# Performance work log

Measured on AMD Instinct MI355X. Metric: run time of the kernel, lower is better.

## Reference

```python
import jax, jax.numpy as jnp
import numpy as np

N_EMBD = 1024
N_HEAD = 16

def setup_inputs() -> dict:
    key = jax.random.key(0)
    ks = jax.random.split(key, 6)
    C = N_EMBD
    s = 1.0 / np.sqrt(C)
    x = jax.random.normal(ks[0], (4, 2048, C), dtype=jnp.float32)
    Wk = jax.random.normal(ks[1], (C, C), dtype=jnp.float32) * s
    Wq = jax.random.normal(ks[2], (C, C), dtype=jnp.float32) * s
    Wv = jax.random.normal(ks[3], (C, C), dtype=jnp.float32) * s
    Wp = jax.random.normal(ks[4], (C, C), dtype=jnp.float32) * s
    bp = jax.random.normal(ks[5], (C,), dtype=jnp.float32) * 0.01
    return {"x": x, "Wq": Wq, "Wk": Wk, "Wv": Wv, "Wp": Wp, "bp": bp}

def reference(x, Wq, Wk, Wv, Wp, bp):
    B, T, C = x.shape
    H = N_HEAD
    d = C // H
    # projections (bias=False)
    q = (x @ Wq).reshape(B, T, H, d).transpose(0, 2, 1, 3)  # [B,H,T,d]
    k = (x @ Wk).reshape(B, T, H, d).transpose(0, 2, 1, 3)
    v = (x @ Wv).reshape(B, T, H, d).transpose(0, 2, 1, 3)
    att = jnp.einsum('bhqd,bhkd->bhqk', q, k) * (1.0 / np.sqrt(d))
    causal = jnp.tril(jnp.ones((T, T), dtype=bool))
    att = jnp.where(causal[None, None], att, jnp.float32(-jnp.inf))
    att = jax.nn.softmax(att, axis=-1)
    y = jnp.einsum('bhqk,bhkd->bhqd', att, v)  # [B,H,T,d]
    y = y.transpose(0, 2, 1, 3).reshape(B, T, C)
    return y @ Wp + bp
```

## Files before the change

### kernel.cpp

```cpp
#include <hip/hip_runtime.h>
#include <hip/hip_bf16.h>

#define N_EMBD 1024
#define N_HEADS 16
#define HD 64
#define TSEQ 2048
#define BATCH 4
#define M_TOT (BATCH*TSEQ)

typedef short s16x8 __attribute__((ext_vector_type(8)));
typedef float f32x4 __attribute__((ext_vector_type(4)));

__device__ __forceinline__ void glds16(const void* g, void* l) {
  __builtin_amdgcn_global_load_lds((const __attribute__((address_space(1))) void*)g,
                                   (__attribute__((address_space(3))) void*)l, 16, 0, 0);
}

__global__ __launch_bounds__(256) void xcast_kernel(const float* __restrict__ x,
                                                    __hip_bfloat16* __restrict__ xb) {
  int i = blockIdx.x * 256 + threadIdx.x;
  float4 f = ((const float4*)x)[i];
  __hip_bfloat162 p0, p1;
  p0.x = __float2bfloat16(f.x); p0.y = __float2bfloat16(f.y);
  p1.x = __float2bfloat16(f.z); p1.y = __float2bfloat16(f.w);
  ((__hip_bfloat162*)xb)[2*i]   = p0;
  ((__hip_bfloat162*)xb)[2*i+1] = p1;
}

__global__ void wcast_kernel(const float* __restrict__ Wq, const float* __restrict__ Wk,
                             const float* __restrict__ Wv, const float* __restrict__ Wp,
                             __hip_bfloat16* __restrict__ wqkvt, __hip_bfloat16* __restrict__ wpt) {
  __shared__ float tile[32][33];
  int z = blockIdx.z;
  const float* in = (z==0)?Wq:(z==1)?Wk:(z==2)?Wv:Wp;
  __hip_bfloat16* out = (z<3) ? (wqkvt + (size_t)z*N_EMBD*N_EMBD) : wpt;
  int tx = threadIdx.x, ty = threadIdx.y;
  int x  = blockIdx.x*32 + tx;
  int y0 = blockIdx.y*32;
  #pragma unroll
  for (int j=0;j<4;++j) tile[ty + j*8][tx] = in[(size_t)(y0+ty+j*8)*N_EMBD + x];
  __syncthreads();
  int xo  = y0 + tx;
  int yo0 = blockIdx.x*32;
  #pragma unroll
  for (int j=0;j<4;++j)
    out[(size_t)(yo0+ty+j*8)*N_EMBD + xo] = __float2bfloat16(tile[tx][ty+j*8]);
}

__global__ __launch_bounds__(256) void gemm_kernel(
    const __hip_bfloat16* __restrict__ A,
    const __hip_bfloat16* __restrict__ Bt,
    __hip_bfloat16* __restrict__ Qb, __hip_bfloat16* __restrict__ Kb,
    __hip_bfloat16* __restrict__ Vt,
    float* __restrict__ out, const float* __restrict__ bias, int mode) {
  __shared__ __align__(16) char smem[32768];
  __hip_bfloat16* Alin = (__hip_bfloat16*)smem;
  __hip_bfloat16* Blin = (__hip_bfloat16*)(smem + 16384);
  int tid = threadIdx.x;
  int m0 = blockIdx.y*128, n0 = blockIdx.x*128;
  int w = tid>>6, lane = tid&63, l16 = lane&15, quad = lane>>4;
  int wr = w>>1, wc = w&1;
  int xg = l16 & 7;
  int off0 = ((quad    ) ^ xg)*8;
  int off1 = ((quad + 4) ^ xg)*8;
  f32x4 acc[4][4];
  #pragma unroll
  for (int mi=0;mi<4;++mi)
    #pragma unroll
    for (int ni=0;ni<4;++ni) acc[mi][ni] = (f32x4){0.f,0.f,0.f,0.f};

  for (int k0=0; k0<N_EMBD; k0+=64) {
    __syncthreads();
    #pragma unroll
    for (int rd=0; rd<4; ++rd) {
      int slot = rd*256 + tid;
      int row  = slot>>3;
      int gc8  = ((tid&7) ^ (row&7))*8;
      glds16(A  + (size_t)(m0+row)*N_EMBD + k0 + gc8, Alin + slot*8);
      glds16(Bt + (size_t)(n0+row)*N_EMBD + k0 + gc8, Blin + slot*8);
    }
    __syncthreads();
    #pragma unroll
    for (int c=0;c<2;++c) {
      int off = c ? off1 : off0;
      s16x8 af[4], bfr[4];
      #pragma unroll
      for (int mi=0;mi<4;++mi)
        af[mi] = *(const s16x8*)(Alin + (wr*64+mi*16+l16)*64 + off);
      #pragma unroll
      for (int ni=0;ni<4;++ni)
        bfr[ni] = *(const s16x8*)(Blin + (wc*64+ni*16+l16)*64 + off);
      #pragma unroll
      for (int mi=0;mi<4;++mi)
        #pragma unroll
        for (int ni=0;ni<4;++ni)
          acc[mi][ni] = __builtin_amdgcn_mfma_f32_16x16x32_bf16(af[mi], bfr[ni], acc[mi][ni],0,0,0);
    }
  }

  if (mode == 0) {
    int which = n0 >> 10;
    int bb = m0 >> 11, t0 = m0 & 2047;
    if (which < 2) {
      __hip_bfloat16* outp = (which==0)?Qb:Kb;
      #pragma unroll
      for (int mi=0;mi<4;++mi) {
        #pragma unroll
        for (int ni=0;ni<4;++ni) {
          int ncol = (n0 & 1023) + wc*64 + ni*16 + l16;
          int hh = ncol>>6, dd = ncol&63;
          #pragma unroll
          for (int r=0;r<4;++r) {
            int t = t0 + wr*64 + mi*16 + quad*4 + r;
            outp[((size_t)(bb*N_HEADS + hh)*TSEQ + t)*HD + dd] = __float2bfloat16(acc[mi][ni][r]);
          }
        }
      }
    } else {
      int hh0 = (n0 & 1023) >> 6;
      __hip_bfloat16 (*Ts)[136] = (__hip_bfloat16(*)[136])smem;
      #pragma unroll
      for (int p=0;p<2;++p) {
        __syncthreads();
        if (wc == p) {
          #pragma unroll
          for (int mi=0;mi<4;++mi)
            #pragma unroll
            for (int ni=0;ni<4;++ni) {
              int dd = ni*16 + l16;
              #pragma unroll
              for (int r=0;r<4;++r)
                Ts[dd][wr*64 + mi*16 + quad*4 + r] = __float2bfloat16(acc[mi][ni][r]);
            }
        }
        __syncthreads();
        int dd = tid>>2, tc = (tid&3)*32;
        __hip_bfloat16* dst = Vt + ((size_t)(bb*N_HEADS + hh0 + p)*HD + dd)*TSEQ + t0 + tc;
        #pragma unroll
        for (int c4=0;c4<4;++c4)
          *(uint4*)(dst + c4*8) = *(const uint4*)&Ts[dd][tc + c4*8];
      }
    }
  } else {
    #pragma unroll
    for (int mi=0;mi<4;++mi) {
      #pragma unroll
      for (int ni=0;ni<4;++ni) {
        int col = n0 + wc*64 + ni*16 + l16;
        float bs = bias[col];
        #pragma unroll
        for (int r=0;r<4;++r) {
          int m = m0 + wr*64 + mi*16 + quad*4 + r;
          out[(size_t)m*N_EMBD + col] = acc[mi][ni][r] + bs;
        }
      }
    }
  }
}

#define PST 68
__global__ __launch_bounds__(256) void attn_kernel(
    const __hip_bfloat16* __restrict__ Qb, const __hip_bfloat16* __restrict__ Kb,
    const __hip_bfloat16* __restrict__ Vt, __hip_bfloat16* __restrict__ Yb) {
  __shared__ __align__(16) __hip_bfloat16 Ks[64][64];
  __shared__ __align__(16) __hip_bfloat16 Vs[64][64];
  __shared__ __align__(16) __hip_bfloat16 Ps[128][PST];
  int tid = threadIdx.x;
  int b = blockIdx.z, h = blockIdx.y;
  int qb = (b & 1) ? (TSEQ/128 - 1 - blockIdx.x) : blockIdx.x;
  int q0 = qb*128;
  size_t bhT  = (size_t)(b*N_HEADS + h)*TSEQ;
  size_t bhHD = (size_t)(b*N_HEADS + h)*HD;
  int lane = tid&63, w = tid>>6, l16 = lane&15, quad = lane>>4;
  int wq = w*32;
  int xg = l16 & 7;
  int off0 = ((quad    ) ^ xg)*8;
  int off1 = ((quad + 4) ^ xg)*8;

  s16x8 qf[2][2];
  #pragma unroll
  for (int mi=0;mi<2;++mi) {
    const __hip_bfloat16* qrow = Qb + (bhT + q0 + wq + mi*16 + l16)*HD;
    qf[mi][0] = *(const s16x8*)(qrow + quad*8);
    qf[mi][1] = *(const s16x8*)(qrow + 32 + quad*8);
  }

  f32x4 z4 = {0.f,0.f,0.f,0.f};
  f32x4 oacc[4][2];
  #pragma unroll
  for (int ni=0;ni<4;++ni) { oacc[ni][0]=z4; oacc[ni][1]=z4; }
  float lrow[2][4] = {{0.f,0.f,0.f,0.f},{0.f,0.f,0.f,0.f}};

  int ntiles = 2*qb + 2;
  for (int t=0; t<ntiles; ++t) {
    int k0 = t*64;
    __syncthreads();
    #pragma unroll
    for (int rd=0; rd<2; ++rd) {
      int slot = rd*256 + tid;
      int row  = slot>>3;
      int gc8  = ((tid&7) ^ (row&7))*8;
      glds16(Kb + (bhT + k0 + row)*HD + gc8,       &Ks[0][0] + slot*8);
      glds16(Vt + (bhHD + row)*TSEQ + k0 + gc8,    &Vs[0][0] + slot*8);
    }
    __syncthreads();

    f32x4 sacc[4][2];
    #pragma unroll
    for (int ni=0; ni<4; ++ni) {
      s16x8 kb0 = *(const s16x8*)(&Ks[0][0] + (ni*16+l16)*64 + off0);
      s16x8 kb1 = *(const s16x8*)(&Ks[0][0] + (ni*16+l16)*64 + off1);
      #pragma unroll
      for (int mi=0; mi<2; ++mi) {
        f32x4 s = z4;
        s = __builtin_amdgcn_mfma_f32_16x16x32_bf16(qf[mi][0], kb0, s,0,0,0);
        s = __builtin_amdgcn_mfma_f32_16x16x32_bf16(qf[mi][1], kb1, s,0,0,0);
        sacc[ni][mi] = s;
      }
    }

    if (q0 + wq >= k0 + 63) {
      #pragma unroll
      for (int ni=0; ni<4; ++ni) {
        #pragma unroll
        for (int mi=0; mi<2; ++mi) {
          #pragma unroll
          for (int r=0; r<4; ++r) {
            float p = __expf(sacc[ni][mi][r]*0.125f);
            lrow[mi][r] += p;
            Ps[wq + mi*16 + quad*4 + r][ni*16 + l16] = __float2bfloat16(p);
          }
        }
      }
    } else {
      #pragma unroll
      for (int ni=0; ni<4; ++ni) {
        int kcol = k0 + ni*16 + l16;
        #pragma unroll
        for (int mi=0; mi<2; ++mi) {
          int qrb = q0 + wq + mi*16 + quad*4;
          #pragma unroll
          for (int r=0; r<4; ++r) {
            float p = (qrb + r >= kcol) ? __expf(sacc[ni][mi][r]*0.125f) : 0.f;
            lrow[mi][r] += p;
            Ps[wq + mi*16 + quad*4 + r][ni*16 + l16] = __float2bfloat16(p);
          }
        }
      }
    }

    union U8 { s16x8 v; uint2 u[2]; };
    U8 aP[2][2];
    #pragma unroll
    for (int mi=0; mi<2; ++mi)
      #pragma unroll
      for (int c=0; c<2; ++c) {
        const __hip_bfloat16* pr = &Ps[wq + mi*16 + l16][c*32 + quad*8];
        aP[mi][c].u[0] = *(const uint2*)pr;
        aP[mi][c].u[1] = *(const uint2*)(pr + 4);
      }
    #pragma unroll
    for (int ni=0; ni<4; ++ni) {
      s16x8 vb0 = *(const s16x8*)(&Vs[0][0] + (ni*16+l16)*64 + off0);
      s16x8 vb1 = *(const s16x8*)(&Vs[0][0] + (ni*16+l16)*64 + off1);
      #pragma unroll
      for (int mi=0; mi<2; ++mi) {
        oacc[ni][mi] = __builtin_amdgcn_mfma_f32_16x16x32_bf16(aP[mi][0].v, vb0, oacc[ni][mi],0,0,0);
        oacc[ni][mi] = __builtin_amdgcn_mfma_f32_16x16x32_bf16(aP[mi][1].v, vb1, oacc[ni][mi],0,0,0);
      }
    }
  }

  #pragma unroll
  for (int off=1; off<16; off<<=1)
    #pragma unroll
    for (int mi=0; mi<2; ++mi)
      #pragma unroll
      for (int r=0; r<4; ++r) lrow[mi][r] += __shfl_xor(lrow[mi][r], off);

  #pragma unroll
  for (int mi=0; mi<2; ++mi)
    #pragma unroll
    for (int r=0; r<4; ++r) {
      float inv = 1.f / lrow[mi][r];
      int tq = q0 + wq + mi*16 + quad*4 + r;
      __hip_bfloat16* yr = Yb + ((size_t)(b*TSEQ + tq))*N_EMBD + h*HD;
      #pragma unroll
      for (int ni=0; ni<4; ++ni)
        yr[ni*16 + l16] = __float2bfloat16(oacc[ni][mi][r] * inv);
    }
}

extern "C" void kernel_launch(void* const* d_in, const int* in_sizes, int n_in,
                              void* d_out, int out_size, void* d_ws, size_t ws_size,
                              hipStream_t stream) {
  const float* x  = (const float*)d_in[0];
  const float* Wq = (const float*)d_in[1];
  const float* Wk = (const float*)d_in[2];
  const float* Wv = (const float*)d_in[3];
  const float* Wp = (const float*)d_in[4];
  const float* bp = (const float*)d_in[5];

  char* w = (char*)d_ws;
  __hip_bfloat16* xb    = (__hip_bfloat16*)w;  w += (size_t)M_TOT*N_EMBD*2;
  __hip_bfloat16* wqkvt = (__hip_bfloat16*)w;  w += (size_t)3*N_EMBD*N_EMBD*2;
  __hip_bfloat16* wpt   = (__hip_bfloat16*)w;  w += (size_t)N_EMBD*N_EMBD*2;
  __hip_bfloat16* Qb    = (__hip_bfloat16*)w;  w += (size_t)M_TOT*N_EMBD*2;
  __hip_bfloat16* Kb    = (__hip_bfloat16*)w;  w += (size_t)M_TOT*N_EMBD*2;
  __hip_bfloat16* Vt    = (__hip_bfloat16*)w;  w += (size_t)M_TOT*N_EMBD*2;
  __hip_bfloat16* Yb    = (__hip_bfloat16*)w;

  xcast_kernel<<<dim3(M_TOT*N_EMBD/1024), dim3(256), 0, stream>>>(x, xb);
  wcast_kernel<<<dim3(32,32,4), dim3(32,8), 0, stream>>>(Wq,Wk,Wv,Wp,wqkvt,wpt);
  gemm_kernel<<<dim3(24,64), dim3(256), 0, stream>>>(xb, wqkvt, Qb,Kb,Vt, nullptr, nullptr, 0);
  attn_kernel<<<dim3(TSEQ/128,N_HEADS,BATCH), dim3(256), 0, stream>>>(Qb,Kb,Vt,Yb);
  gemm_kernel<<<dim3(8,64), dim3(256), 0, stream>>>(Yb, wpt, nullptr,nullptr,nullptr,
                                                    (float*)d_out, bp, 1);
}
```

Before: 281.9 us.

## Double-buffer K/V tiles in attention with async LDS prefetch

Makes the K and V shared-memory tiles double-buffered and issues the global-to-LDS loads for the next tile before computing on the current one. Explicit vmcnt waits and raw barriers replace the two __syncthreads per tile, with a closing barrier to protect buffer reuse. The aim is to hide global load latency behind the MFMA and softmax work. In exchange it doubles K/V LDS use, which may lower occupancy, and it relies on hand-written waitcnt correctness.

```diff
diff --git a/kernel.cpp b/kernel.cpp
--- a/kernel.cpp
+++ b/kernel.cpp
@@ -162,8 +162,8 @@
 __global__ __launch_bounds__(256) void attn_kernel(
     const __hip_bfloat16* __restrict__ Qb, const __hip_bfloat16* __restrict__ Kb,
     const __hip_bfloat16* __restrict__ Vt, __hip_bfloat16* __restrict__ Yb) {
-  __shared__ __align__(16) __hip_bfloat16 Ks[64][64];
-  __shared__ __align__(16) __hip_bfloat16 Vs[64][64];
+  __shared__ __align__(16) __hip_bfloat16 Ks[2][64][64];
+  __shared__ __align__(16) __hip_bfloat16 Vs[2][64][64];
   __shared__ __align__(16) __hip_bfloat16 Ps[128][PST];
   int tid = threadIdx.x;
   int b = blockIdx.z, h = blockIdx.y;
@@ -177,6 +177,9 @@
   int off0 = ((quad    ) ^ xg)*8;
   int off1 = ((quad + 4) ^ xg)*8;
 
+  int slot0 = tid,        row0 = slot0>>3, gcA = ((tid&7) ^ (row0&7))*8;
+  int slot1 = 256 + tid,  row1 = slot1>>3, gcB = ((tid&7) ^ (row1&7))*8;
+
   s16x8 qf[2][2];
   #pragma unroll
   for (int mi=0;mi<2;++mi) {
@@ -192,24 +195,38 @@
   float lrow[2][4] = {{0.f,0.f,0.f,0.f},{0.f,0.f,0.f,0.f}};
 
   int ntiles = 2*qb + 2;
+
+  {
+    glds16(Kb + (bhT + 0 + row0)*HD + gcA,    &Ks[0][0][0] + slot0*8);
+    glds16(Vt + (bhHD + row0)*TSEQ + 0 + gcA, &Vs[0][0][0] + slot0*8);
+    glds16(Kb + (bhT + 0 + row1)*HD + gcB,    &Ks[0][0][0] + slot1*8);
+    glds16(Vt + (bhHD + row1)*TSEQ + 0 + gcB, &Vs[0][0][0] + slot1*8);
+  }
+
   for (int t=0; t<ntiles; ++t) {
+    int cur = t&1;
     int k0 = t*64;
-    __syncthreads();
-    #pragma unroll
-    for (int rd=0; rd<2; ++rd) {
-      int slot = rd*256 + tid;
-      int row  = slot>>3;
-      int gc8  = ((tid&7) ^ (row&7))*8;
-      glds16(Kb + (bhT + k0 + row)*HD + gc8,       &Ks[0][0] + slot*8);
-      glds16(Vt + (bhHD + row)*TSEQ + k0 + gc8,    &Vs[0][0] + slot*8);
-    }
-    __syncthreads();
+    if (t+1 < ntiles) {
+      int kn = k0 + 64;
+      glds16(Kb + (bhT + kn + row0)*HD + gcA,     &Ks[cur^1][0][0] + slot0*8);
+      glds16(Vt + (bhHD + row0)*TSEQ + kn + gcA,  &Vs[cur^1][0][0] + slot0*8);
+      glds16(Kb + (bhT + kn + row1)*HD + gcB,     &Ks[cur^1][0][0] + slot1*8);
+      glds16(Vt + (bhHD + row1)*TSEQ + kn + gcB,  &Vs[cur^1][0][0] + slot1*8);
+      asm volatile("s_waitcnt vmcnt(4)" ::: "memory");
+    } else {
+      asm volatile("s_waitcnt vmcnt(0)" ::: "memory");
+    }
+    __builtin_amdgcn_s_barrier();
+    __builtin_amdgcn_sched_barrier(0);
+
+    const __hip_bfloat16* Kc = &Ks[cur][0][0];
+    const __hip_bfloat16* Vc = &Vs[cur][0][0];
 
     f32x4 sacc[4][2];
     #pragma unroll
     for (int ni=0; ni<4; ++ni) {
-      s16x8 kb0 = *(const s16x8*)(&Ks[0][0] + (ni*16+l16)*64 + off0);
-      s16x8 kb1 = *(const s16x8*)(&Ks[0][0] + (ni*16+l16)*64 + off1);
+      s16x8 kb0 = *(const s16x8*)(Kc + (ni*16+l16)*64 + off0);
+      s16x8 kb1 = *(const s16x8*)(Kc + (ni*16+l16)*64 + off1);
       #pragma unroll
       for (int mi=0; mi<2; ++mi) {
         f32x4 s = z4;
@@ -261,14 +278,18 @@
       }
     #pragma unroll
     for (int ni=0; ni<4; ++ni) {
-      s16x8 vb0 = *(const s16x8*)(&Vs[0][0] + (ni*16+l16)*64 + off0);
-      s16x8 vb1 = *(const s16x8*)(&Vs[0][0] + (ni*16+l16)*64 + off1);
+      s16x8 vb0 = *(const s16x8*)(Vc + (ni*16+l16)*64 + off0);
+      s16x8 vb1 = *(const s16x8*)(Vc + (ni*16+l16)*64 + off1);
       #pragma unroll
       for (int mi=0; mi<2; ++mi) {
         oacc[ni][mi] = __builtin_amdgcn_mfma_f32_16x16x32_bf16(aP[mi][0].v, vb0, oacc[ni][mi],0,0,0);
         oacc[ni][mi] = __builtin_amdgcn_mfma_f32_16x16x32_bf16(aP[mi][1].v, vb1, oacc[ni][mi],0,0,0);
       }
     }
+
+    asm volatile("s_waitcnt lgkmcnt(0)" ::: "memory");
+    __builtin_amdgcn_s_barrier();
+    __builtin_amdgcn_sched_barrier(0);
   }
 
   #pragma unroll
```

Result: no change. 278.4 us (-1.2%).
